# Performance work log

Hardware: AMD Instinct MI355X
Metric: run time of the kernel (lower is better)

## Reference

```python
import jax, jax.numpy as jnp
import numpy as np

B, N, K, S = 4, 50000, 128, 256  # batch, correspondences, num_subsets, num_samples
EPS = 1e-5


def setup_inputs() -> dict:
    key = jax.random.key(0)
    k1, k2, k3, k4 = jax.random.split(key, 4)
    src = jax.random.normal(k1, (B, N, 3), jnp.float32)
    tgt = jax.random.normal(k2, (B, N, 3), jnp.float32)
    w = jax.random.uniform(k3, (B, N), jnp.float32)
    sel = jax.random.randint(k4, (K, S), 0, N)
    return {"src_corr_points": src, "tgt_corr_points": tgt,
            "corr_weights": w, "sel_indices": sel}


def weighted_procrustes(src, tgt, w):
    """src,tgt: (M,S,3); w: (M,S) -> (M,4,4) rigid transforms (Kabsch/Umeyama)."""
    w = w / (jnp.sum(w, axis=1, keepdims=True) + EPS)
    w3 = w[..., None]  # (M,S,1)
    src_c = jnp.sum(src * w3, axis=1, keepdims=True)  # (M,1,3)
    tgt_c = jnp.sum(tgt * w3, axis=1, keepdims=True)
    src0 = src - src_c
    tgt0 = tgt - tgt_c
    H = jnp.einsum('msi,msj->mij', src0, w3 * tgt0)  # (M,3,3)
    Uu, _, Vh = jnp.linalg.svd(H)
    V = jnp.swapaxes(Vh, -1, -2)
    Ut = jnp.swapaxes(Uu, -1, -2)
    det = jnp.linalg.det(jnp.matmul(V, Ut))
    d = jnp.stack([jnp.ones_like(det), jnp.ones_like(det), jnp.sign(det)], axis=-1)
    R = jnp.matmul(V * d[:, None, :], Ut)  # (M,3,3)
    t = tgt_c[:, 0, :] - jnp.einsum('mij,mj->mi', R, src_c[:, 0, :])  # (M,3)
    M = R.shape[0]
    T = jnp.zeros((M, 4, 4), R.dtype)
    T = T.at[:, :3, :3].set(R).at[:, :3, 3].set(t).at[:, 3, 3].set(1.0)
    return T


def reference(src_corr_points, tgt_corr_points, corr_weights, sel_indices):
    b, n = corr_weights.shape
    k, s = sel_indices.shape
    # random-subset gather -> (b*k, s, 3) / (b*k, s)
    sel_src = src_corr_points[:, sel_indices, :].reshape(b * k, s, 3)
    sel_tgt = tgt_corr_points[:, sel_indices, :].reshape(b * k, s, 3)
    sel_w = corr_weights[:, sel_indices].reshape(b * k, s)
    transforms = weighted_procrustes(sel_src, sel_tgt, sel_w)  # (b*k,4,4)
    Tb = transforms.reshape(b, k, 4, 4)
    R = Tb[:, :, :3, :3]  # (b,k,3,3)
    t = Tb[:, :, :3, 3]   # (b,k,3)
    # apply all k hypotheses to all n src points: (b,k,n,3)
    aligned = jnp.einsum('bkij,bnj->bkni', R, src_corr_points) + t[:, :, None, :]
    diff = aligned - tgt_corr_points[:, None, :, :]
    corr_errors = jnp.linalg.norm(diff, axis=-1)  # (b,k,n)
    weighted_errors = jnp.mean(corr_errors * corr_weights[:, None, :], axis=2)  # (b,k)
    best = jnp.argmin(weighted_errors, axis=1)  # (b,)
    best_transform = Tb[jnp.arange(b), best]  # (b,4,4)
    return best_transform
```

## Files before the change

kernel.cpp:

```cpp
#include <hip/hip_runtime.h>
#include <hip/hip_bf16.h>

constexpr int B = 4;
constexpr int N = 50000;
constexpr int K = 128;
constexpr int S = 256;
constexpr int NCH = (N + 255) / 256;
constexpr float EPS = 1e-5f;

__device__ __forceinline__ float frcp  (float x) { return __builtin_amdgcn_rcpf(x); }
__device__ __forceinline__ float frsq  (float x) { return __builtin_amdgcn_rsqf(x); }
__device__ __forceinline__ float fsqrt_(float x) { return __builtin_amdgcn_sqrtf(x); }

template<int P, int Q>
__device__ __forceinline__ void rot(float (&A)[4][4], float (&V)[4][4])
{
  const float apq = A[P][Q];
  const float theta = 0.5f * (A[Q][Q] - A[P][P]) * frcp(apq);
  const float tt = copysignf(
      frcp(fabsf(theta) + fsqrt_(fmaf(theta, theta, 1.f))), theta);
  float c  = frsq(fmaf(tt, tt, 1.f));
  float sn = tt * c;
  const bool tiny = fabsf(apq) < 1e-20f;
  c  = tiny ? 1.f : c;
  sn = tiny ? 0.f : sn;
  #pragma unroll
  for (int i = 0; i < 4; ++i) {
    const float aip = A[i][P], aiq = A[i][Q];
    A[i][P] = c * aip - sn * aiq;
    A[i][Q] = sn * aip + c * aiq;
  }
  #pragma unroll
  for (int i = 0; i < 4; ++i) {
    const float api = A[P][i], aqi = A[Q][i];
    A[P][i] = c * api - sn * aqi;
    A[Q][i] = sn * api + c * aqi;
  }
  #pragma unroll
  for (int i = 0; i < 4; ++i) {
    const float vip = V[i][P], viq = V[i][Q];
    V[i][P] = c * vip - sn * viq;
    V[i][Q] = sn * vip + c * viq;
  }
}

__device__ __forceinline__ void solve_and_write(const float (&Sm)[16], float* To)
{
  const float W   = Sm[0];
  const float inv = frcp(W + EPS);
  const float scx = Sm[1]*inv, scy = Sm[2]*inv, scz = Sm[3]*inv;
  const float tcx = Sm[4]*inv, tcy = Sm[5]*inv, tcz = Sm[6]*inv;
  const float f = 2.f - W * inv;
  const float Sxx = Sm[7]*inv  - f*scx*tcx;
  const float Sxy = Sm[8]*inv  - f*scx*tcy;
  const float Sxz = Sm[9]*inv  - f*scx*tcz;
  const float Syx = Sm[10]*inv - f*scy*tcx;
  const float Syy = Sm[11]*inv - f*scy*tcy;
  const float Syz = Sm[12]*inv - f*scy*tcz;
  const float Szx = Sm[13]*inv - f*scz*tcx;
  const float Szy = Sm[14]*inv - f*scz*tcy;
  const float Szz = Sm[15]*inv - f*scz*tcz;

  float A[4][4], V[4][4];
  A[0][0] = Sxx + Syy + Szz;
  A[0][1] = Syz - Szy;  A[0][2] = Szx - Sxz;  A[0][3] = Sxy - Syx;
  A[1][1] = Sxx - Syy - Szz;
  A[1][2] = Sxy + Syx;  A[1][3] = Szx + Sxz;
  A[2][2] = -Sxx + Syy - Szz;
  A[2][3] = Syz + Szy;
  A[3][3] = -Sxx - Syy + Szz;
  A[1][0] = A[0][1]; A[2][0] = A[0][2]; A[3][0] = A[0][3];
  A[2][1] = A[1][2]; A[3][1] = A[1][3]; A[3][2] = A[2][3];

  #pragma unroll
  for (int i = 0; i < 4; ++i)
    #pragma unroll
    for (int j = 0; j < 4; ++j) V[i][j] = (i == j) ? 1.f : 0.f;

  #pragma unroll 1
  for (int sweep = 0; sweep < 5; ++sweep) {
    rot<0,1>(A, V); rot<0,2>(A, V); rot<0,3>(A, V);
    rot<1,2>(A, V); rot<1,3>(A, V); rot<2,3>(A, V);
  }

  const float d0 = A[0][0], d1 = A[1][1], d2 = A[2][2], d3 = A[3][3];
  const bool b1 = d1 > d0;
  const bool b3 = d3 > d2;
  const bool bb = (b3 ? d3 : d2) > (b1 ? d1 : d0);
  float qw  = bb ? (b3 ? V[0][3] : V[0][2]) : (b1 ? V[0][1] : V[0][0]);
  float qxv = bb ? (b3 ? V[1][3] : V[1][2]) : (b1 ? V[1][1] : V[1][0]);
  float qyv = bb ? (b3 ? V[2][3] : V[2][2]) : (b1 ? V[2][1] : V[2][0]);
  float qzv = bb ? (b3 ? V[3][3] : V[3][2]) : (b1 ? V[3][1] : V[3][0]);

  const float qn = frsq(qw*qw + qxv*qxv + qyv*qyv + qzv*qzv);
  qw *= qn; qxv *= qn; qyv *= qn; qzv *= qn;

  const float R00 = 1.f - 2.f*(qyv*qyv + qzv*qzv);
  const float R01 = 2.f*(qxv*qyv - qw*qzv);
  const float R02 = 2.f*(qxv*qzv + qw*qyv);
  const float R10 = 2.f*(qxv*qyv + qw*qzv);
  const float R11 = 1.f - 2.f*(qxv*qxv + qzv*qzv);
  const float R12 = 2.f*(qyv*qzv - qw*qxv);
  const float R20 = 2.f*(qxv*qzv - qw*qyv);
  const float R21 = 2.f*(qyv*qzv + qw*qxv);
  const float R22 = 1.f - 2.f*(qxv*qxv + qyv*qyv);

  const float tx = tcx - (R00*scx + R01*scy + R02*scz);
  const float ty = tcy - (R10*scx + R11*scy + R12*scz);
  const float tz = tcz - (R20*scx + R21*scy + R22*scz);

  float4* T4 = (float4*)To;
  T4[0] = make_float4(R00, R01, R02, tx);
  T4[1] = make_float4(R10, R11, R12, ty);
  T4[2] = make_float4(R20, R21, R22, tz);
  T4[3] = make_float4(0.f, 0.f, 0.f, 1.f);
}

__global__ __launch_bounds__(256) void gather_solve_kernel(
    const float* __restrict__ src, const float* __restrict__ tgt,
    const float* __restrict__ wts, const int* __restrict__ sel,
    float* __restrict__ T)
{
  const int bid = blockIdx.x;
  const int xcd = bid & 7;
  const int b   = xcd >> 1;
  const int k   = ((bid >> 3) << 1) | (xcd & 1);
  const int s   = threadIdx.x;

  const int idx = sel[k * S + s];
  const float* ps = src + (size_t)(b * N + idx) * 3;
  const float* pt = tgt + (size_t)(b * N + idx) * 3;
  const float w  = wts[b * N + idx];
  const float px = ps[0], py = ps[1], pz = ps[2];
  const float qx = pt[0], qy = pt[1], qz = pt[2];

  float acc[16];
  acc[0] = w;
  acc[1] = w * px;  acc[2] = w * py;  acc[3] = w * pz;
  acc[4] = w * qx;  acc[5] = w * qy;  acc[6] = w * qz;
  acc[7]  = w * px * qx; acc[8]  = w * px * qy; acc[9]  = w * px * qz;
  acc[10] = w * py * qx; acc[11] = w * py * qy; acc[12] = w * py * qz;
  acc[13] = w * pz * qx; acc[14] = w * pz * qy; acc[15] = w * pz * qz;

  #pragma unroll
  for (int off = 32; off > 0; off >>= 1) {
    #pragma unroll
    for (int i = 0; i < 16; ++i)
      acc[i] += __shfl_down(acc[i], off);
  }

  __shared__ float red[4][16];
  const int lane = threadIdx.x & 63, wv = threadIdx.x >> 6;
  if (lane == 0) {
    #pragma unroll
    for (int i = 0; i < 16; ++i) red[wv][i] = acc[i];
  }
  __syncthreads();

  if (threadIdx.x == 0) {
    float Sm[16];
    #pragma unroll
    for (int i = 0; i < 16; ++i)
      Sm[i] = red[0][i] + red[1][i] + red[2][i] + red[3][i];
    solve_and_write(Sm, T + (size_t)(b * K + k) * 16);
  }
}

constexpr int KPT = 4;
constexpr int KG  = K / KPT;
constexpr int NSL = 256 / KG;
constexpr int PPS = 256 / NSL;

__global__ __launch_bounds__(256) void error_kernel(
    const float* __restrict__ src, const float* __restrict__ tgt,
    const float* __restrict__ wts, const float* __restrict__ T,
    float* __restrict__ partial)
{
  __shared__ float4 sp[256];
  __shared__ float4 sq[256];
  __shared__ float  t4[K][12];
  __shared__ float  red[K][NSL + 1];

  const int bid = blockIdx.x;
  const int xcd = bid & 7;
  const int b   = xcd >> 1;
  const int ch  = ((bid >> 3) << 1) | (xcd & 1);
  const int tid = threadIdx.x;
  const int j   = ch * 256 + tid;

  float4 P = make_float4(0.f, 0.f, 0.f, 0.f);
  float4 Q = make_float4(0.f, 0.f, 0.f, 0.f);
  if (j < N) {
    const float* ps = src + (size_t)(b*N + j) * 3;
    const float* pt = tgt + (size_t)(b*N + j) * 3;
    P.x = ps[0]; P.y = ps[1]; P.z = ps[2]; P.w = wts[b*N + j];
    Q.x = pt[0]; Q.y = pt[1]; Q.z = pt[2];
  }
  sp[tid] = P; sq[tid] = Q;

  if (tid < K) {
    const float* tp = T + (size_t)(b*K + tid) * 16;
    #pragma unroll
    for (int c = 0; c < 12; ++c) t4[tid][c] = tp[c];
  }
  __syncthreads();

  const int kg    = tid & (KG - 1);
  const int slice = tid >> 5;

  float R[KPT][12];
  #pragma unroll
  for (int m = 0; m < KPT; ++m) {
    const int k = kg + m * KG;
    #pragma unroll
    for (int c = 0; c < 12; ++c) R[m][c] = t4[k][c];
  }

  float acc[KPT] = {0.f, 0.f, 0.f, 0.f};
  const int base = slice * PPS;
  #pragma unroll 4
  for (int i = 0; i < PPS; ++i) {
    const float4 p = sp[base + i];
    const float4 q = sq[base + i];
    #pragma unroll
    for (int m = 0; m < KPT; ++m) {
      const float dx = fmaf(R[m][0], p.x, fmaf(R[m][1], p.y, fmaf(R[m][2],  p.z, R[m][3])))  - q.x;
      const float dy = fmaf(R[m][4], p.x, fmaf(R[m][5], p.y, fmaf(R[m][6],  p.z, R[m][7])))  - q.y;
      const float dz = fmaf(R[m][8], p.x, fmaf(R[m][9], p.y, fmaf(R[m][10], p.z, R[m][11]))) - q.z;
      const float d2 = fmaf(dx, dx, fmaf(dy, dy, dz*dz));
      acc[m] = fmaf(p.w, fsqrt_(d2), acc[m]);
    }
  }

  #pragma unroll
  for (int m = 0; m < KPT; ++m)
    red[kg + m * KG][slice] = acc[m];
  __syncthreads();

  if (tid < K) {
    float sum = 0.f;
    #pragma unroll
    for (int s2 = 0; s2 < NSL; ++s2) sum += red[tid][s2];
    partial[((size_t)b * NCH + ch) * K + tid] = sum;
  }
}

__global__ __launch_bounds__(256) void argmin_kernel(
    const float* __restrict__ partial, const float* __restrict__ T,
    float* __restrict__ out)
{
  const int b   = blockIdx.x;
  const int tid = threadIdx.x;
  const int k   = tid & (K - 1);
  const int h   = tid >> 7;

  float sum = 0.f;
  #pragma unroll 7
  for (int c = h; c < NCH; c += 2)
    sum += partial[((size_t)b * NCH + c) * K + k];

  __shared__ float vals[256];
  __shared__ int   idxs[K];
  vals[tid] = sum;
  __syncthreads();

  if (tid < K) { vals[tid] = vals[tid] + vals[tid + K]; idxs[tid] = tid; }
  __syncthreads();

  for (int off = K / 2; off > 0; off >>= 1) {
    if (tid < off) {
      const float o = vals[tid + off];
      if (o < vals[tid] || (o == vals[tid] && idxs[tid + off] < idxs[tid])) {
        vals[tid] = o; idxs[tid] = idxs[tid + off];
      }
    }
    __syncthreads();
  }

  const int best = idxs[0];
  if (tid < 16) out[(size_t)b * 16 + tid] = T[(size_t)(b * K + best) * 16 + tid];
}

extern "C" void kernel_launch(void* const* d_in, const int* in_sizes, int n_in,
                              void* d_out, int out_size, void* d_ws, size_t ws_size,
                              hipStream_t stream) {
  const float* src = (const float*)d_in[0];
  const float* tgt = (const float*)d_in[1];
  const float* wts = (const float*)d_in[2];
  const int*   sel = (const int*)d_in[3];

  float* T       = (float*)d_ws;
  float* partial = T + (size_t)B * K * 16;

  gather_solve_kernel<<<B * K, 256, 0, stream>>>(src, tgt, wts, sel, T);
  error_kernel<<<B * NCH, 256, 0, stream>>>(src, tgt, wts, T, partial);
  argmin_kernel<<<B, 256, 0, stream>>>(partial, T, (float*)d_out);
}
```

Baseline: 43.89 us.

## Bucket selected indices by point chunk and accumulate Procrustes moments per chunk

Replaces the random per-hypothesis gather with a pipeline of its own. The selected indices are scattered into buckets by point chunk, then each chunk's points are loaded into shared memory and the 16 weighted moments are accumulated per hypothesis with LDS atomics. A reduction kernel then sums the chunk partials and solves each transform. The aim is to turn scattered global reads into coalesced chunk loads, at the cost of three extra launches, a memset, atomic contention, and a fixed bucket capacity that could overflow and drop entries.

Result: slower. 113.8 us (+159.3%).

```diff
diff --git a/kernel.cpp b/kernel.cpp
--- a/kernel.cpp
+++ b/kernel.cpp
@@ -6,6 +6,9 @@
 constexpr int K = 128;
 constexpr int S = 256;
 constexpr int NCH = (N + 255) / 256;
+constexpr int CH   = 64;
+constexpr int CPTS = 782;
+constexpr int CAP  = 1024;
 constexpr float EPS = 1e-5f;
 
 __device__ __forceinline__ float frcp  (float x) { return __builtin_amdgcn_rcpf(x); }
@@ -116,6 +119,117 @@
   T4[3] = make_float4(0.f, 0.f, 0.f, 1.f);
 }
 
+__global__ __launch_bounds__(256) void scatter_kernel(
+    const int* __restrict__ sel, unsigned* __restrict__ bucket,
+    int* __restrict__ cnt)
+{
+  const int e = blockIdx.x * 256 + threadIdx.x;
+  const int k   = e >> 8;
+  const int idx = sel[e];
+  const int c   = idx / CPTS;
+  const int slot = atomicAdd(&cnt[c], 1);
+  if (slot < CAP)
+    bucket[c * CAP + slot] = ((unsigned)k << 16) | (unsigned)idx;
+}
+
+__global__ __launch_bounds__(256) void moment_kernel(
+    const float* __restrict__ src, const float* __restrict__ tgt,
+    const float* __restrict__ wts, const unsigned* __restrict__ bucket,
+    const int* __restrict__ cnt, float* __restrict__ part)
+{
+  __shared__ float4 sp[CPTS];
+  __shared__ float4 sq[CPTS];
+  __shared__ float  mom[K * 17];
+
+  const int bid = blockIdx.x;
+  const int xcd = bid & 7;
+  const int b   = xcd >> 1;
+  const int c   = ((bid >> 3) << 1) | (xcd & 1);
+  const int tid = threadIdx.x;
+
+  const int lo = c * CPTS;
+  const int cp = min(CPTS, N - lo);
+
+  for (int i = tid; i < cp; i += 256) {
+    const int p = b * N + lo + i;
+    sp[i] = make_float4(src[3*p], src[3*p+1], src[3*p+2], wts[p]);
+    sq[i] = make_float4(tgt[3*p], tgt[3*p+1], tgt[3*p+2], 0.f);
+  }
+  for (int t = tid; t < K * 17; t += 256) mom[t] = 0.f;
+  __syncthreads();
+
+  const int nb = min(cnt[c], CAP);
+  for (int e = tid; e < nb; e += 256) {
+    const unsigned u = bucket[c * CAP + e];
+    const int k = (int)(u >> 16);
+    const int d = (int)(u & 0xFFFFu) - lo;
+    const float4 P = sp[d];
+    const float4 Q = sq[d];
+    const float w = P.w;
+    float* m = &mom[k * 17];
+    atomicAdd(m + 0,  w);
+    atomicAdd(m + 1,  w * P.x);
+    atomicAdd(m + 2,  w * P.y);
+    atomicAdd(m + 3,  w * P.z);
+    atomicAdd(m + 4,  w * Q.x);
+    atomicAdd(m + 5,  w * Q.y);
+    atomicAdd(m + 6,  w * Q.z);
+    const float wx = w * P.x, wy = w * P.y, wz = w * P.z;
+    atomicAdd(m + 7,  wx * Q.x);
+    atomicAdd(m + 8,  wx * Q.y);
+    atomicAdd(m + 9,  wx * Q.z);
+    atomicAdd(m + 10, wy * Q.x);
+    atomicAdd(m + 11, wy * Q.y);
+    atomicAdd(m + 12, wy * Q.z);
+    atomicAdd(m + 13, wz * Q.x);
+    atomicAdd(m + 14, wz * Q.y);
+    atomicAdd(m + 15, wz * Q.z);
+  }
+  __syncthreads();
+
+  float* out = part + (size_t)(b * CH + c) * (K * 16);
+  for (int t = tid; t < K * 16; t += 256)
+    out[t] = mom[(t >> 4) * 17 + (t & 15)];
+}
+
+__global__ __launch_bounds__(256) void reduce_solve_kernel(
+    const float* __restrict__ part, float* __restrict__ T)
+{
+  const int bid = blockIdx.x;
+  const int b   = bid >> 7;
+  const int k   = bid & (K - 1);
+  const int tid = threadIdx.x;
+  const int i   = tid & 15;
+  const int sg  = tid >> 4;
+
+  float sum = 0.f;
+  #pragma unroll
+  for (int m = 0; m < CH / 16; ++m) {
+    const int c = sg + 16 * m;
+    sum += part[(size_t)(b * CH + c) * (K * 16) + k * 16 + i];
+  }
+
+  __shared__ float red[16][17];
+  red[sg][i] = sum;
+  __syncthreads();
+
+  __shared__ float SmS[16];
+  if (tid < 16) {
+    float t = 0.f;
+    #pragma unroll
+    for (int g = 0; g < 16; ++g) t += red[g][tid];
+    SmS[tid] = t;
+  }
+  __syncthreads();
+
+  if (tid == 0) {
+    float Sm[16];
+    #pragma unroll
+    for (int z = 0; z < 16; ++z) Sm[z] = SmS[z];
+    solve_and_write(Sm, T + (size_t)(b * K + k) * 16);
+  }
+}
+
 __global__ __launch_bounds__(256) void gather_solve_kernel(
     const float* __restrict__ src, const float* __restrict__ tgt,
     const float* __restrict__ wts, const int* __restrict__ sel,
@@ -289,10 +403,33 @@
   const float* wts = (const float*)d_in[2];
   const int*   sel = (const int*)d_in[3];
 
-  float* T       = (float*)d_ws;
-  float* partial = T + (size_t)B * K * 16;
-
-  gather_solve_kernel<<<B * K, 256, 0, stream>>>(src, tgt, wts, sel, T);
-  error_kernel<<<B * NCH, 256, 0, stream>>>(src, tgt, wts, T, partial);
-  argmin_kernel<<<B, 256, 0, stream>>>(partial, T, (float*)d_out);
-}
+  const size_t cnt_bytes    = 256;
+  const size_t bucket_bytes = (size_t)CH * CAP * 4;
+  const size_t part_floats  = (size_t)B * CH * K * 16;
+  const size_t T_floats     = (size_t)B * K * 16;
+  const size_t partial_floats = (size_t)B * NCH * K;
+  const size_t need = cnt_bytes + bucket_bytes +
+      (part_floats + T_floats + partial_floats) * sizeof(float);
+
+  if (ws_size >= need) {
+    int*      cnt    = (int*)d_ws;
+    unsigned* bucket = (unsigned*)((char*)d_ws + cnt_bytes);
+    float*    part   = (float*)((char*)d_ws + cnt_bytes + bucket_bytes);
+    float*    T      = part + part_floats;
+    float*    partial = T + T_floats;
+
+    hipMemsetAsync(cnt, 0, CH * sizeof(int), stream);
+    scatter_kernel<<<(K * S) / 256, 256, 0, stream>>>(sel, bucket, cnt);
+    moment_kernel<<<B * CH, 256, 0, stream>>>(src, tgt, wts, bucket, cnt, part);
+    reduce_solve_kernel<<<B * K, 256, 0, stream>>>(part, T);
+    error_kernel<<<B * NCH, 256, 0, stream>>>(src, tgt, wts, T, partial);
+    argmin_kernel<<<B, 256, 0, stream>>>(partial, T, (float*)d_out);
+  } else {
+    float* T       = (float*)d_ws;
+    float* partial = T + T_floats;
+
+    gather_solve_kernel<<<B * K, 256, 0, stream>>>(src, tgt, wts, sel, T);
+    error_kernel<<<B * NCH, 256, 0, stream>>>(src, tgt, wts, T, partial);
+    argmin_kernel<<<B, 256, 0, stream>>>(partial, T, (float*)d_out);
+  }
+}
```

## Split gather reduction from eigen-solve into separate per-thread solve kernel

Applied to the files above, without the earlier changes.

Separates the per-hypothesis moment reduction from the quaternion Jacobi eigen-solve. The reduction blocks now just write 16 sums, and a new small kernel runs one solve per thread across 512 lanes instead of one lone thread per 256-thread block. The Jacobi rotation is also rewritten to update only the symmetric upper-triangle entries as scalars, cutting arithmetic and register use. This adds a kernel launch and a round-trip of the sums through global memory, in exchange for removing the serial single-thread tail from each gather block.

Result: faster. 37.18 us (-15.3%).

```diff
diff --git a/kernel.cpp b/kernel.cpp
--- a/kernel.cpp
+++ b/kernel.cpp
@@ -12,11 +12,62 @@
 __device__ __forceinline__ float frsq  (float x) { return __builtin_amdgcn_rsqf(x); }
 __device__ __forceinline__ float fsqrt_(float x) { return __builtin_amdgcn_sqrtf(x); }
 
-template<int P, int Q>
-__device__ __forceinline__ void rot(float (&A)[4][4], float (&V)[4][4])
-{
-  const float apq = A[P][Q];
-  const float theta = 0.5f * (A[Q][Q] - A[P][P]) * frcp(apq);
+__global__ __launch_bounds__(256) void gather_sums_kernel(
+    const float* __restrict__ src, const float* __restrict__ tgt,
+    const float* __restrict__ wts, const int* __restrict__ sel,
+    float* __restrict__ sums)
+{
+  const int bid = blockIdx.x;
+  const int xcd = bid & 7;
+  const int b   = xcd >> 1;
+  const int k   = ((bid >> 3) << 1) | (xcd & 1);
+  const int s   = threadIdx.x;
+
+  const int idx = sel[k * S + s];
+  const float* ps = src + (size_t)(b * N + idx) * 3;
+  const float* pt = tgt + (size_t)(b * N + idx) * 3;
+  const float w  = wts[b * N + idx];
+  const float px = ps[0], py = ps[1], pz = ps[2];
+  const float qx = pt[0], qy = pt[1], qz = pt[2];
+
+  float acc[16];
+  acc[0] = w;
+  acc[1] = w * px;  acc[2] = w * py;  acc[3] = w * pz;
+  acc[4] = w * qx;  acc[5] = w * qy;  acc[6] = w * qz;
+  acc[7]  = w * px * qx; acc[8]  = w * px * qy; acc[9]  = w * px * qz;
+  acc[10] = w * py * qx; acc[11] = w * py * qy; acc[12] = w * py * qz;
+  acc[13] = w * pz * qx; acc[14] = w * pz * qy; acc[15] = w * pz * qz;
+
+  #pragma unroll
+  for (int off = 32; off > 0; off >>= 1) {
+    #pragma unroll
+    for (int i = 0; i < 16; ++i)
+      acc[i] += __shfl_down(acc[i], off);
+  }
+
+  __shared__ float red[4][16];
+  const int lane = threadIdx.x & 63, wv = threadIdx.x >> 6;
+  if (lane == 0) {
+    #pragma unroll
+    for (int i = 0; i < 16; ++i) red[wv][i] = acc[i];
+  }
+  __syncthreads();
+
+  if (threadIdx.x < 16) {
+    const int i = threadIdx.x;
+    sums[(size_t)(b * K + k) * 16 + i] =
+        red[0][i] + red[1][i] + red[2][i] + red[3][i];
+  }
+}
+
+__device__ __forceinline__ void jrot(
+    float& app, float& apq, float& aqq,
+    float& ar1p, float& ar1q,
+    float& ar2p, float& ar2q,
+    float& v0p, float& v0q, float& v1p, float& v1q,
+    float& v2p, float& v2q, float& v3p, float& v3q)
+{
+  const float theta = 0.5f * (aqq - app) * frcp(apq);
   const float tt = copysignf(
       frcp(fabsf(theta) + fsqrt_(fmaf(theta, theta, 1.f))), theta);
   float c  = frsq(fmaf(tt, tt, 1.f));
@@ -24,73 +75,82 @@
   const bool tiny = fabsf(apq) < 1e-20f;
   c  = tiny ? 1.f : c;
   sn = tiny ? 0.f : sn;
-  #pragma unroll
-  for (int i = 0; i < 4; ++i) {
-    const float aip = A[i][P], aiq = A[i][Q];
-    A[i][P] = c * aip - sn * aiq;
-    A[i][Q] = sn * aip + c * aiq;
-  }
-  #pragma unroll
-  for (int i = 0; i < 4; ++i) {
-    const float api = A[P][i], aqi = A[Q][i];
-    A[P][i] = c * api - sn * aqi;
-    A[Q][i] = sn * api + c * aqi;
-  }
-  #pragma unroll
-  for (int i = 0; i < 4; ++i) {
-    const float vip = V[i][P], viq = V[i][Q];
-    V[i][P] = c * vip - sn * viq;
-    V[i][Q] = sn * vip + c * viq;
-  }
-}
-
-__device__ __forceinline__ void solve_and_write(const float (&Sm)[16], float* To)
-{
-  const float W   = Sm[0];
+
+  const float cc = c * c, ss = sn * sn, cs = c * sn;
+  const float app_ = cc * app - 2.f * cs * apq + ss * aqq;
+  const float aqq_ = ss * app + 2.f * cs * apq + cc * aqq;
+  apq = (cc - ss) * apq + cs * (app - aqq);
+  app = app_;  aqq = aqq_;
+
+  float t;
+  t = c * ar1p - sn * ar1q;  ar1q = sn * ar1p + c * ar1q;  ar1p = t;
+  t = c * ar2p - sn * ar2q;  ar2q = sn * ar2p + c * ar2q;  ar2p = t;
+
+  t = c * v0p - sn * v0q;  v0q = sn * v0p + c * v0q;  v0p = t;
+  t = c * v1p - sn * v1q;  v1q = sn * v1p + c * v1q;  v1p = t;
+  t = c * v2p - sn * v2q;  v2q = sn * v2p + c * v2q;  v2p = t;
+  t = c * v3p - sn * v3q;  v3q = sn * v3p + c * v3q;  v3p = t;
+}
+
+__global__ __launch_bounds__(64) void solve_kernel(
+    const float* __restrict__ sums, float* __restrict__ T)
+{
+  const int bk = blockIdx.x * 64 + threadIdx.x;
+
+  const float4* s4 = (const float4*)(sums + (size_t)bk * 16);
+  const float4 sA = s4[0], sB = s4[1], sC = s4[2], sD = s4[3];
+
+  const float W   = sA.x;
   const float inv = frcp(W + EPS);
-  const float scx = Sm[1]*inv, scy = Sm[2]*inv, scz = Sm[3]*inv;
-  const float tcx = Sm[4]*inv, tcy = Sm[5]*inv, tcz = Sm[6]*inv;
+  const float scx = sA.y * inv, scy = sA.z * inv, scz = sA.w * inv;
+  const float tcx = sB.x * inv, tcy = sB.y * inv, tcz = sB.z * inv;
   const float f = 2.f - W * inv;
-  const float Sxx = Sm[7]*inv  - f*scx*tcx;
-  const float Sxy = Sm[8]*inv  - f*scx*tcy;
-  const float Sxz = Sm[9]*inv  - f*scx*tcz;
-  const float Syx = Sm[10]*inv - f*scy*tcx;
-  const float Syy = Sm[11]*inv - f*scy*tcy;
-  const float Syz = Sm[12]*inv - f*scy*tcz;
-  const float Szx = Sm[13]*inv - f*scz*tcx;
-  const float Szy = Sm[14]*inv - f*scz*tcy;
-  const float Szz = Sm[15]*inv - f*scz*tcz;
-
-  float A[4][4], V[4][4];
-  A[0][0] = Sxx + Syy + Szz;
-  A[0][1] = Syz - Szy;  A[0][2] = Szx - Sxz;  A[0][3] = Sxy - Syx;
-  A[1][1] = Sxx - Syy - Szz;
-  A[1][2] = Sxy + Syx;  A[1][3] = Szx + Sxz;
-  A[2][2] = -Sxx + Syy - Szz;
-  A[2][3] = Syz + Szy;
-  A[3][3] = -Sxx - Syy + Szz;
-  A[1][0] = A[0][1]; A[2][0] = A[0][2]; A[3][0] = A[0][3];
-  A[2][1] = A[1][2]; A[3][1] = A[1][3]; A[3][2] = A[2][3];
-
-  #pragma unroll
-  for (int i = 0; i < 4; ++i)
-    #pragma unroll
-    for (int j = 0; j < 4; ++j) V[i][j] = (i == j) ? 1.f : 0.f;
+  const float Sxx = sB.w * inv - f * scx * tcx;
+  const float Sxy = sC.x * inv - f * scx * tcy;
+  const float Sxz = sC.y * inv - f * scx * tcz;
+  const float Syx = sC.z * inv - f * scy * tcx;
+  const float Syy = sC.w * inv - f * scy * tcy;
+  const float Syz = sD.x * inv - f * scy * tcz;
+  const float Szx = sD.y * inv - f * scz * tcx;
+  const float Szy = sD.z * inv - f * scz * tcy;
+  const float Szz = sD.w * inv - f * scz * tcz;
+
+  float a00 = Sxx + Syy + Szz;
+  float a01 = Syz - Szy,  a02 = Szx - Sxz,  a03 = Sxy - Syx;
+  float a11 = Sxx - Syy - Szz;
+  float a12 = Sxy + Syx,  a13 = Szx + Sxz;
+  float a22 = -Sxx + Syy - Szz;
+  float a23 = Syz + Szy;
+  float a33 = -Sxx - Syy + Szz;
+
+  float v00 = 1.f, v01 = 0.f, v02 = 0.f, v03 = 0.f;
+  float v10 = 0.f, v11 = 1.f, v12 = 0.f, v13 = 0.f;
+  float v20 = 0.f, v21 = 0.f, v22 = 1.f, v23 = 0.f;
+  float v30 = 0.f, v31 = 0.f, v32 = 0.f, v33 = 1.f;
 
   #pragma unroll 1
   for (int sweep = 0; sweep < 5; ++sweep) {
-    rot<0,1>(A, V); rot<0,2>(A, V); rot<0,3>(A, V);
-    rot<1,2>(A, V); rot<1,3>(A, V); rot<2,3>(A, V);
-  }
-
-  const float d0 = A[0][0], d1 = A[1][1], d2 = A[2][2], d3 = A[3][3];
-  const bool b1 = d1 > d0;
-  const bool b3 = d3 > d2;
-  const bool bb = (b3 ? d3 : d2) > (b1 ? d1 : d0);
-  float qw  = bb ? (b3 ? V[0][3] : V[0][2]) : (b1 ? V[0][1] : V[0][0]);
-  float qxv = bb ? (b3 ? V[1][3] : V[1][2]) : (b1 ? V[1][1] : V[1][0]);
-  float qyv = bb ? (b3 ? V[2][3] : V[2][2]) : (b1 ? V[2][1] : V[2][0]);
-  float qzv = bb ? (b3 ? V[3][3] : V[3][2]) : (b1 ? V[3][1] : V[3][0]);
+    jrot(a00, a01, a11, a02, a12, a03, a13,
+         v00, v01, v10, v11, v20, v21, v30, v31);
+    jrot(a00, a02, a22, a01, a12, a03, a23,
+         v00, v02, v10, v12, v20, v22, v30, v32);
+    jrot(a00, a03, a33, a01, a13, a02, a23,
+         v00, v03, v10, v13, v20, v23, v30, v33);
+    jrot(a11, a12, a22, a01, a02, a13, a23,
+         v01, v02, v11, v12, v21, v22, v31, v32);
+    jrot(a11, a13, a33, a01, a03, a12, a23,
+         v01, v03, v11, v13, v21, v23, v31, v33);
+    jrot(a22, a23, a33, a02, a03, a12, a13,
+         v02, v03, v12, v13, v22, v23, v32, v33);
+  }
+
+  const bool b1 = a11 > a00;
+  const bool b3 = a33 > a22;
+  const bool bb = (b3 ? a33 : a22) > (b1 ? a11 : a00);
+  float qw  = bb ? (b3 ? v03 : v02) : (b1 ? v01 : v00);
+  float qxv = bb ? (b3 ? v13 : v12) : (b1 ? v11 : v10);
+  float qyv = bb ? (b3 ? v23 : v22) : (b1 ? v21 : v20);
+  float qzv = bb ? (b3 ? v33 : v32) : (b1 ? v31 : v30);
 
   const float qn = frsq(qw*qw + qxv*qxv + qyv*qyv + qzv*qzv);
   qw *= qn; qxv *= qn; qyv *= qn; qzv *= qn;
@@ -109,61 +169,11 @@
   const float ty = tcy - (R10*scx + R11*scy + R12*scz);
   const float tz = tcz - (R20*scx + R21*scy + R22*scz);
 
-  float4* T4 = (float4*)To;
+  float4* T4 = (float4*)(T + (size_t)bk * 16);
   T4[0] = make_float4(R00, R01, R02, tx);
   T4[1] = make_float4(R10, R11, R12, ty);
   T4[2] = make_float4(R20, R21, R22, tz);
   T4[3] = make_float4(0.f, 0.f, 0.f, 1.f);
-}
-
-__global__ __launch_bounds__(256) void gather_solve_kernel(
-    const float* __restrict__ src, const float* __restrict__ tgt,
-    const float* __restrict__ wts, const int* __restrict__ sel,
-    float* __restrict__ T)
-{
-  const int bid = blockIdx.x;
-  const int xcd = bid & 7;
-  const int b   = xcd >> 1;
-  const int k   = ((bid >> 3) << 1) | (xcd & 1);
-  const int s   = threadIdx.x;
-
-  const int idx = sel[k * S + s];
-  const float* ps = src + (size_t)(b * N + idx) * 3;
-  const float* pt = tgt + (size_t)(b * N + idx) * 3;
-  const float w  = wts[b * N + idx];
-  const float px = ps[0], py = ps[1], pz = ps[2];
-  const float qx = pt[0], qy = pt[1], qz = pt[2];
-
-  float acc[16];
-  acc[0] = w;
-  acc[1] = w * px;  acc[2] = w * py;  acc[3] = w * pz;
-  acc[4] = w * qx;  acc[5] = w * qy;  acc[6] = w * qz;
-  acc[7]  = w * px * qx; acc[8]  = w * px * qy; acc[9]  = w * px * qz;
-  acc[10] = w * py * qx; acc[11] = w * py * qy; acc[12] = w * py * qz;
-  acc[13] = w * pz * qx; acc[14] = w * pz * qy; acc[15] = w * pz * qz;
-
-  #pragma unroll
-  for (int off = 32; off > 0; off >>= 1) {
-    #pragma unroll
-    for (int i = 0; i < 16; ++i)
-      acc[i] += __shfl_down(acc[i], off);
-  }
-
-  __shared__ float red[4][16];
-  const int lane = threadIdx.x & 63, wv = threadIdx.x >> 6;
-  if (lane == 0) {
-    #pragma unroll
-    for (int i = 0; i < 16; ++i) red[wv][i] = acc[i];
-  }
-  __syncthreads();
-
-  if (threadIdx.x == 0) {
-    float Sm[16];
-    #pragma unroll
-    for (int i = 0; i < 16; ++i)
-      Sm[i] = red[0][i] + red[1][i] + red[2][i] + red[3][i];
-    solve_and_write(Sm, T + (size_t)(b * K + k) * 16);
-  }
 }
 
 constexpr int KPT = 4;
@@ -289,10 +299,12 @@
   const float* wts = (const float*)d_in[2];
   const int*   sel = (const int*)d_in[3];
 
-  float* T       = (float*)d_ws;
+  float* sums    = (float*)d_ws;
+  float* T       = sums + (size_t)B * K * 16;
   float* partial = T + (size_t)B * K * 16;
 
-  gather_solve_kernel<<<B * K, 256, 0, stream>>>(src, tgt, wts, sel, T);
+  gather_sums_kernel<<<B * K, 256, 0, stream>>>(src, tgt, wts, sel, sums);
+  solve_kernel<<<8, 64, 0, stream>>>(sums, T);
   error_kernel<<<B * NCH, 256, 0, stream>>>(src, tgt, wts, T, partial);
   argmin_kernel<<<B, 256, 0, stream>>>(partial, T, (float*)d_out);
 }
```
